# Kernel optimization log

Measured on AMD Instinct MI355X. Metric: run time of the kernel, lower is better.

Reference implementation:

```python
import jax, jax.numpy as jnp
import numpy as np

N_NODES = 50000
N_EDGES = 800000
IN_CH = 128
OUT_CH = 64
HEADS = 4
NEG_SLOPE = 0.2


def setup_inputs() -> dict:
    key = jax.random.key(0)
    k1, k2, k3, k4, k5 = jax.random.split(key, 5)
    x = jax.random.normal(k1, (N_NODES, IN_CH), dtype=jnp.float32)
    edge_index = jax.random.randint(k2, (2, N_EDGES), 0, N_NODES, dtype=jnp.int64)
    # Glorot-ish scaled params
    W = jax.random.normal(k3, (IN_CH, HEADS * OUT_CH), dtype=jnp.float32) * (1.0 / np.sqrt(IN_CH))
    att_src = jax.random.normal(k4, (HEADS, OUT_CH), dtype=jnp.float32) * (1.0 / np.sqrt(OUT_CH))
    att_dst = jax.random.normal(k5, (HEADS, OUT_CH), dtype=jnp.float32) * (1.0 / np.sqrt(OUT_CH))
    bias = jnp.zeros((HEADS * OUT_CH,), dtype=jnp.float32)
    return {"x": x, "edge_index": edge_index, "W": W, "att_src": att_src, "att_dst": att_dst, "bias": bias}


def reference(x, edge_index, W, att_src, att_dst, bias):
    N = x.shape[0]
    H, C = att_src.shape
    # PyG GATConv default add_self_loops=True
    loops = jnp.arange(N, dtype=edge_index.dtype)
    src = jnp.concatenate([edge_index[0], loops])  # message source j
    dst = jnp.concatenate([edge_index[1], loops])  # message target i
    # Linear transform per head: [N, H, C]
    h = (x @ W).reshape(N, H, C)
    # Per-node attention logits: [N, H]
    a_src = jnp.sum(h * att_src[None], axis=-1)
    a_dst = jnp.sum(h * att_dst[None], axis=-1)
    # Per-edge raw score (alpha_src from source node, alpha_dst from target node)
    e = jax.nn.leaky_relu(a_src[src] + a_dst[dst], NEG_SLOPE)  # [E, H]
    # Segment-softmax over incoming edges of each target node
    m = jax.ops.segment_max(e, dst, num_segments=N)  # [N, H]
    m = jnp.where(jnp.isfinite(m), m, 0.0)  # nodes with no edges -> 0
    ex = jnp.exp(e - m[dst])
    denom = jax.ops.segment_sum(ex, dst, num_segments=N)  # [N, H]
    alpha = ex / (denom[dst] + 1e-16)  # [E, H]
    # Weighted aggregate of source features: [N, H, C]
    msg = h[src] * alpha[:, :, None]
    out = jax.ops.segment_sum(msg, dst, num_segments=N)
    # concat=True: flatten heads, add bias
    return out.reshape(N, H * C) + bias
```

## Files before the change

kernel.cpp:

```cpp
#include <hip/hip_runtime.h>

#define N_NODES 50000
#define N_EDGES 800000
#define IN_CH 128
#define OUT_CH 64
#define HEADS 4
#define HC 256
#define NEG_SLOPE 0.2f
#define GEMM_BLOCKS 782
#define COUNT_BLOCKS 782
#define SCAN_BLOCKS 49

#define HB_OFF       0UL
#define WSW_OFF      25600000UL
#define ASRC_OFF     25665536UL
#define ADST_OFF     26465536UL
#define COUNTS_OFF   27265536UL
#define OFFSETS_OFF  27465536UL
#define BSUMS_OFF    27665536UL
#define RANK_OFF     27666560UL
#define SIDX_OFF     30866560UL
#define EXV_OFF      34066560UL

typedef __attribute__((ext_vector_type(8))) short short8;
typedef __attribute__((ext_vector_type(8))) __fp16 f16x8;
typedef __attribute__((ext_vector_type(4))) unsigned uint32x4;
typedef __attribute__((ext_vector_type(4))) float f32x4;
typedef __attribute__((ext_vector_type(2))) __fp16 fp16x2;

__device__ __forceinline__ unsigned f2h2(float a, float b) {
  fp16x2 h = __builtin_amdgcn_cvt_pkrtz(a, b);
  return __builtin_bit_cast(unsigned, h);
}
__device__ __forceinline__ void fma2(float& a0, float& a1, unsigned u, float e) {
  fp16x2 h = __builtin_bit_cast(fp16x2, u);
  a0 = fmaf((float)h.x, e, a0);
  a1 = fmaf((float)h.y, e, a1);
}
__device__ __forceinline__ float lrelu(float e) {
  return e > 0.f ? e : NEG_SLOPE * e;
}

__global__ __launch_bounds__(256) void init_k(const float* __restrict__ W,
                                              unsigned short* __restrict__ Wsw,
                                              int* __restrict__ counts) {
  if (blockIdx.x < 16) {
    int idx = blockIdx.x * 256 + threadIdx.x;
    int l = idx & 63;
    int kc = (idx >> 6) & 3;
    int t = idx >> 8;
    int kbase = kc * 32 + (l >> 4) * 8;
    int col = t * 16 + (l & 15);
    unsigned int p[4];
#pragma unroll
    for (int j = 0; j < 4; ++j) {
      p[j] = f2h2(W[(size_t)(kbase + 2 * j) * HC + col],
                  W[(size_t)(kbase + 2 * j + 1) * HC + col]);
    }
    *(uint4*)(Wsw + (size_t)idx * 8) = make_uint4(p[0], p[1], p[2], p[3]);
  } else {
    int i = (blockIdx.x - 16) * 256 + threadIdx.x;
    if (i < N_NODES) counts[i] = 0;
  }
}

__global__ __launch_bounds__(256) void gemm_count(const float* __restrict__ x,
                                                  const unsigned short* __restrict__ Wsw,
                                                  const float* __restrict__ att_s,
                                                  const float* __restrict__ att_d,
                                                  const int* __restrict__ dstv,
                                                  unsigned short* __restrict__ hb,
                                                  float* __restrict__ a_src,
                                                  float* __restrict__ a_dst,
                                                  int* __restrict__ counts,
                                                  int* __restrict__ rank) {
  __shared__ float Cs[4][16][256];

  if (blockIdx.x >= GEMM_BLOCKS) {
    int base = (blockIdx.x - GEMM_BLOCKS) * 1024 + threadIdx.x;
#pragma unroll
    for (int k = 0; k < 4; ++k) {
      int e = base + k * 256;
      if (e < N_EDGES) rank[e] = atomicAdd(&counts[dstv[e]], 1);
    }
    return;
  }

  const int wave = threadIdx.x >> 6;
  const int l = threadIdx.x & 63;
  const int q = l >> 4;
  const int m = l & 15;
  const int mrow = blockIdx.x * 64 + wave * 16 + m;
  const bool mvalid = mrow < N_NODES;
  const int rc = mvalid ? mrow : (N_NODES - 1);

  f16x8 a[4];
  const float* xr = x + (size_t)rc * IN_CH + q * 8;
#pragma unroll
  for (int kc = 0; kc < 4; ++kc) {
    float4 u = *(const float4*)(xr + kc * 32);
    float4 v = *(const float4*)(xr + kc * 32 + 4);
    uint32x4 t;
    t[0] = f2h2(u.x, u.y);
    t[1] = f2h2(u.z, u.w);
    t[2] = f2h2(v.x, v.y);
    t[3] = f2h2(v.z, v.w);
    a[kc] = __builtin_bit_cast(f16x8, t);
  }

#pragma unroll
  for (int t = 0; t < 16; ++t) {
    f32x4 acc = {0.f, 0.f, 0.f, 0.f};
#pragma unroll
    for (int kc = 0; kc < 4; ++kc) {
      f16x8 b = *(const f16x8*)(Wsw + ((size_t)(t * 4 + kc) * 64 + l) * 8);
      acc = __builtin_amdgcn_mfma_f32_16x16x32_f16(a[kc], b, acc, 0, 0, 0);
    }
#pragma unroll
    for (int r = 0; r < 4; ++r) {
      int row = q * 4 + r;
      Cs[wave][row][(t * 16 + m) ^ (row << 2)] = acc[r];
    }
  }
  __syncthreads();

  float as = 0.f, ad = 0.f;
  unsigned short* hrow = hb + (size_t)mrow * HC + q * 64;
  const int sw = m << 2;
#pragma unroll
  for (int i = 0; i < 8; ++i) {
    int col0 = q * 64 + i * 8;
    float4 c1 = *(const float4*)&Cs[wave][m][(col0) ^ sw];
    float4 c2 = *(const float4*)&Cs[wave][m][(col0 + 4) ^ sw];
    float4 s1 = *(const float4*)(att_s + col0);
    float4 s2 = *(const float4*)(att_s + col0 + 4);
    float4 d1 = *(const float4*)(att_d + col0);
    float4 d2 = *(const float4*)(att_d + col0 + 4);
    as += c1.x * s1.x + c1.y * s1.y + c1.z * s1.z + c1.w * s1.w;
    as += c2.x * s2.x + c2.y * s2.y + c2.z * s2.z + c2.w * s2.w;
    ad += c1.x * d1.x + c1.y * d1.y + c1.z * d1.z + c1.w * d1.w;
    ad += c2.x * d2.x + c2.y * d2.y + c2.z * d2.z + c2.w * d2.w;
    if (mvalid) {
      uint4 p;
      p.x = f2h2(c1.x, c1.y);
      p.y = f2h2(c1.z, c1.w);
      p.z = f2h2(c2.x, c2.y);
      p.w = f2h2(c2.z, c2.w);
      *(uint4*)(hrow + i * 8) = p;
    }
  }
  if (mvalid) {
    a_src[mrow * HEADS + q] = as;
    a_dst[mrow * HEADS + q] = ad;
  }
}

__global__ __launch_bounds__(256) void scan1(const int* __restrict__ counts,
                                             int* __restrict__ offsets,
                                             int* __restrict__ bsums) {
  __shared__ int sd[256];
  const int base = blockIdx.x * 1024;
  const int t = threadIdx.x;
  int v[4];
  int tsum = 0;
#pragma unroll
  for (int k = 0; k < 4; ++k) {
    int i = base + t * 4 + k;
    v[k] = (i < N_NODES) ? counts[i] : 0;
    tsum += v[k];
  }
  sd[t] = tsum;
  __syncthreads();
  for (int off = 1; off < 256; off <<= 1) {
    int xval = (t >= off) ? sd[t - off] : 0;
    __syncthreads();
    sd[t] += xval;
    __syncthreads();
  }
  int excl = sd[t] - tsum;
  int run = excl;
#pragma unroll
  for (int k = 0; k < 4; ++k) {
    int i = base + t * 4 + k;
    if (i < N_NODES) offsets[i] = run;
    run += v[k];
  }
  if (t == 255) bsums[blockIdx.x] = sd[255];
}

__global__ __launch_bounds__(256) void scan23(int* __restrict__ offsets,
                                              const int* __restrict__ bsums) {
  __shared__ int s_add;
  if (threadIdx.x < 64) {
    int lane = threadIdx.x;
    int v = (lane < SCAN_BLOCKS) ? bsums[lane] : 0;
#pragma unroll
    for (int o = 1; o < 64; o <<= 1) {
      int t = __shfl_up(v, o);
      if (lane >= o) v += t;
    }
    int b = blockIdx.x;
    int pre = (b == 0) ? 0 : __shfl(v, b - 1);
    if (lane == 0) s_add = pre;
  }
  __syncthreads();
  const int add = s_add;
  const int base = blockIdx.x * 1024;
  const int t = threadIdx.x;
#pragma unroll
  for (int k = 0; k < 4; ++k) {
    int i = base + t * 4 + k;
    if (i < N_NODES) offsets[i] += add;
  }
}

__global__ __launch_bounds__(256) void scatter_k(const int* __restrict__ src,
                                                 const int* __restrict__ dst,
                                                 const int* __restrict__ rank,
                                                 const int* __restrict__ offsets,
                                                 const float* __restrict__ a_src,
                                                 const float* __restrict__ a_dst,
                                                 int* __restrict__ sidx,
                                                 float* __restrict__ exv) {
  int e = blockIdx.x * 256 + threadIdx.x;
  if (e < N_EDGES) {
    int s = src[e];
    int d = dst[e];
    float4 as = *(const float4*)(a_src + s * 4);
    float4 ad = *(const float4*)(a_dst + d * 4);
    float4 ex;
    ex.x = __expf(lrelu(as.x + ad.x));
    ex.y = __expf(lrelu(as.y + ad.y));
    ex.z = __expf(lrelu(as.z + ad.z));
    ex.w = __expf(lrelu(as.w + ad.w));
    int pos = offsets[d] + rank[e];
    sidx[pos] = s;
    *(float4*)(exv + (size_t)pos * 4) = ex;
  }
}

__global__ __launch_bounds__(256) void aggregate(const unsigned short* __restrict__ hb,
                                                 const float* __restrict__ a_src,
                                                 const float* __restrict__ a_dst,
                                                 const int* __restrict__ counts,
                                                 const int* __restrict__ offsets,
                                                 const int* __restrict__ sidx,
                                                 const float* __restrict__ exv,
                                                 const float* __restrict__ bias,
                                                 float* __restrict__ out) {
  const int node = blockIdx.x * 4 + (threadIdx.x >> 6);
  const int l = threadIdx.x & 63;
  const int g = l >> 4;
  const int q = l & 15;
  const int hd = q >> 2;
  const int cb = q * 32;
  const int deg = counts[node];
  const int start = offsets[node];
  const char* hbase = (const char*)hb;

  float denom = 0.f;
  float acc[16];
#pragma unroll
  for (int k = 0; k < 16; ++k) acc[k] = 0.f;

  for (int j = 0; j + g < deg; j += 8) {
    int i0 = start + j + g;
    bool v1 = (j + g + 4) < deg;
    int i1 = v1 ? (i0 + 4) : i0;
    int s0 = sidx[i0];
    int s1 = sidx[i1];
    float ex0 = exv[(size_t)i0 * 4 + hd];
    float ex1 = v1 ? exv[(size_t)i1 * 4 + hd] : 0.f;
    const char* hp0 = hbase + (size_t)s0 * 512 + cb;
    const char* hp1 = hbase + (size_t)s1 * 512 + cb;
    uint4 A0 = *(const uint4*)hp0;
    uint4 A1 = *(const uint4*)(hp0 + 16);
    uint4 B0 = *(const uint4*)hp1;
    uint4 B1 = *(const uint4*)(hp1 + 16);
    denom += ex0 + ex1;
    fma2(acc[0],  acc[1],  A0.x, ex0);  fma2(acc[2],  acc[3],  A0.y, ex0);
    fma2(acc[4],  acc[5],  A0.z, ex0);  fma2(acc[6],  acc[7],  A0.w, ex0);
    fma2(acc[8],  acc[9],  A1.x, ex0);  fma2(acc[10], acc[11], A1.y, ex0);
    fma2(acc[12], acc[13], A1.z, ex0);  fma2(acc[14], acc[15], A1.w, ex0);
    fma2(acc[0],  acc[1],  B0.x, ex1);  fma2(acc[2],  acc[3],  B0.y, ex1);
    fma2(acc[4],  acc[5],  B0.z, ex1);  fma2(acc[6],  acc[7],  B0.w, ex1);
    fma2(acc[8],  acc[9],  B1.x, ex1);  fma2(acc[10], acc[11], B1.y, ex1);
    fma2(acc[12], acc[13], B1.z, ex1);  fma2(acc[14], acc[15], B1.w, ex1);
  }

  denom += __shfl_xor(denom, 16);
  denom += __shfl_xor(denom, 32);
#pragma unroll
  for (int k = 0; k < 16; ++k) {
    acc[k] += __shfl_xor(acc[k], 16);
    acc[k] += __shfl_xor(acc[k], 32);
  }

  float es = a_src[node * HEADS + hd] + a_dst[node * HEADS + hd];
  float exs = __expf(lrelu(es));
  denom += exs;
  const char* hp = hbase + (size_t)node * 512 + cb;
  uint4 h0 = *(const uint4*)hp;
  uint4 h1 = *(const uint4*)(hp + 16);
  fma2(acc[0],  acc[1],  h0.x, exs);  fma2(acc[2],  acc[3],  h0.y, exs);
  fma2(acc[4],  acc[5],  h0.z, exs);  fma2(acc[6],  acc[7],  h0.w, exs);
  fma2(acc[8],  acc[9],  h1.x, exs);  fma2(acc[10], acc[11], h1.y, exs);
  fma2(acc[12], acc[13], h1.z, exs);  fma2(acc[14], acc[15], h1.w, exs);

  float inv = 1.f / (denom + 1e-16f);
  int c = q * 16 + g * 4;
  float4 bv = *(const float4*)(bias + c);
  float4 o = make_float4(acc[g * 4 + 0] * inv + bv.x, acc[g * 4 + 1] * inv + bv.y,
                         acc[g * 4 + 2] * inv + bv.z, acc[g * 4 + 3] * inv + bv.w);
  *(float4*)(out + (size_t)node * HC + c) = o;
}

extern "C" void kernel_launch(void* const* d_in, const int* in_sizes, int n_in,
                              void* d_out, int out_size, void* d_ws, size_t ws_size,
                              hipStream_t stream) {
  const float* x     = (const float*)d_in[0];
  const int*   ei    = (const int*)d_in[1];
  const float* W     = (const float*)d_in[2];
  const float* att_s = (const float*)d_in[3];
  const float* att_d = (const float*)d_in[4];
  const float* bias  = (const float*)d_in[5];
  float* out = (float*)d_out;

  char* ws = (char*)d_ws;
  unsigned short* hb  = (unsigned short*)(ws + HB_OFF);
  unsigned short* Wsw = (unsigned short*)(ws + WSW_OFF);
  float* a_src  = (float*)(ws + ASRC_OFF);
  float* a_dst  = (float*)(ws + ADST_OFF);
  int* counts   = (int*)(ws + COUNTS_OFF);
  int* offsets  = (int*)(ws + OFFSETS_OFF);
  int* bsums    = (int*)(ws + BSUMS_OFF);
  int* rank     = (int*)(ws + RANK_OFF);
  int* sidx     = (int*)(ws + SIDX_OFF);
  float* exv    = (float*)(ws + EXV_OFF);

  const int* src = ei;
  const int* dst = ei + N_EDGES;

  init_k<<<16 + 196, 256, 0, stream>>>(W, Wsw, counts);
  gemm_count<<<GEMM_BLOCKS + COUNT_BLOCKS, 256, 0, stream>>>(
      x, Wsw, att_s, att_d, dst, hb, a_src, a_dst, counts, rank);
  scan1<<<SCAN_BLOCKS, 256, 0, stream>>>(counts, offsets, bsums);
  scan23<<<SCAN_BLOCKS, 256, 0, stream>>>(offsets, bsums);
  scatter_k<<<3125, 256, 0, stream>>>(src, dst, rank, offsets, a_src, a_dst, sidx, exv);
  aggregate<<<12500, 256, 0, stream>>>(hb, a_src, a_dst, counts, offsets, sidx, exv, bias, out);
}
```

Baseline: 233.5 us.

## Pack per-edge index and fp16 exp weights into one record; halve GEMM LDS tile

The scatter stage now writes one 16-byte record per edge, holding the source index plus the four per-head exp weights packed as fp16, in place of separate index and float4 arrays. Aggregate then reads a single uint4 per edge instead of two scattered loads. The GEMM epilogue is split into two passes over half-width shared-memory tiles, halving LDS use per block to raise occupancy, at the cost of an extra barrier. Storing the exp weights in fp16 loses precision and can overflow for large logits, since there is no max subtraction.

Result: faster. 224.8 us (-3.7%).

```diff
diff --git a/kernel.cpp b/kernel.cpp
--- a/kernel.cpp
+++ b/kernel.cpp
@@ -19,10 +19,8 @@
 #define OFFSETS_OFF  27465536UL
 #define BSUMS_OFF    27665536UL
 #define RANK_OFF     27666560UL
-#define SIDX_OFF     30866560UL
-#define EXV_OFF      34066560UL
-
-typedef __attribute__((ext_vector_type(8))) short short8;
+#define REC_OFF      30866560UL
+
 typedef __attribute__((ext_vector_type(8))) __fp16 f16x8;
 typedef __attribute__((ext_vector_type(4))) unsigned uint32x4;
 typedef __attribute__((ext_vector_type(4))) float f32x4;
@@ -39,6 +37,11 @@
 }
 __device__ __forceinline__ float lrelu(float e) {
   return e > 0.f ? e : NEG_SLOPE * e;
+}
+__device__ __forceinline__ float exhalf(uint4 r, int hd) {
+  unsigned pair = (hd & 2) ? r.z : r.y;
+  fp16x2 h = __builtin_bit_cast(fp16x2, pair);
+  return (hd & 1) ? (float)h.y : (float)h.x;
 }
 
 __global__ __launch_bounds__(256) void init_k(const float* __restrict__ W,
@@ -74,7 +77,7 @@
                                                   float* __restrict__ a_dst,
                                                   int* __restrict__ counts,
                                                   int* __restrict__ rank) {
-  __shared__ float Cs[4][16][256];
+  __shared__ float Cs[4][16][128];
 
   if (blockIdx.x >= GEMM_BLOCKS) {
     int base = (blockIdx.x - GEMM_BLOCKS) * 1024 + threadIdx.x;
@@ -108,45 +111,52 @@
     a[kc] = __builtin_bit_cast(f16x8, t);
   }
 
-#pragma unroll
-  for (int t = 0; t < 16; ++t) {
-    f32x4 acc = {0.f, 0.f, 0.f, 0.f};
-#pragma unroll
-    for (int kc = 0; kc < 4; ++kc) {
-      f16x8 b = *(const f16x8*)(Wsw + ((size_t)(t * 4 + kc) * 64 + l) * 8);
-      acc = __builtin_amdgcn_mfma_f32_16x16x32_f16(a[kc], b, acc, 0, 0, 0);
-    }
-#pragma unroll
-    for (int r = 0; r < 4; ++r) {
-      int row = q * 4 + r;
-      Cs[wave][row][(t * 16 + m) ^ (row << 2)] = acc[r];
-    }
-  }
-  __syncthreads();
-
   float as = 0.f, ad = 0.f;
   unsigned short* hrow = hb + (size_t)mrow * HC + q * 64;
   const int sw = m << 2;
-#pragma unroll
-  for (int i = 0; i < 8; ++i) {
-    int col0 = q * 64 + i * 8;
-    float4 c1 = *(const float4*)&Cs[wave][m][(col0) ^ sw];
-    float4 c2 = *(const float4*)&Cs[wave][m][(col0 + 4) ^ sw];
-    float4 s1 = *(const float4*)(att_s + col0);
-    float4 s2 = *(const float4*)(att_s + col0 + 4);
-    float4 d1 = *(const float4*)(att_d + col0);
-    float4 d2 = *(const float4*)(att_d + col0 + 4);
-    as += c1.x * s1.x + c1.y * s1.y + c1.z * s1.z + c1.w * s1.w;
-    as += c2.x * s2.x + c2.y * s2.y + c2.z * s2.z + c2.w * s2.w;
-    ad += c1.x * d1.x + c1.y * d1.y + c1.z * d1.z + c1.w * d1.w;
-    ad += c2.x * d2.x + c2.y * d2.y + c2.z * d2.z + c2.w * d2.w;
-    if (mvalid) {
-      uint4 p;
-      p.x = f2h2(c1.x, c1.y);
-      p.y = f2h2(c1.z, c1.w);
-      p.z = f2h2(c2.x, c2.y);
-      p.w = f2h2(c2.z, c2.w);
-      *(uint4*)(hrow + i * 8) = p;
+
+#pragma unroll
+  for (int P = 0; P < 2; ++P) {
+    if (P) __syncthreads();
+#pragma unroll
+    for (int tt = 0; tt < 8; ++tt) {
+      int t = ((tt >> 1) << 2) + P * 2 + (tt & 1);
+      f32x4 acc = {0.f, 0.f, 0.f, 0.f};
+#pragma unroll
+      for (int kc = 0; kc < 4; ++kc) {
+        f16x8 b = *(const f16x8*)(Wsw + ((size_t)(t * 4 + kc) * 64 + l) * 8);
+        acc = __builtin_amdgcn_mfma_f32_16x16x32_f16(a[kc], b, acc, 0, 0, 0);
+      }
+#pragma unroll
+      for (int r = 0; r < 4; ++r) {
+        int row = q * 4 + r;
+        Cs[wave][row][(tt * 16 + m) ^ (row << 2)] = acc[r];
+      }
+    }
+    __syncthreads();
+
+#pragma unroll
+    for (int i = 0; i < 4; ++i) {
+      int lcol = q * 32 + i * 8;
+      float4 c1 = *(const float4*)&Cs[wave][m][(lcol) ^ sw];
+      float4 c2 = *(const float4*)&Cs[wave][m][(lcol + 4) ^ sw];
+      int ch = q * 64 + P * 32 + i * 8;
+      float4 s1 = *(const float4*)(att_s + ch);
+      float4 s2 = *(const float4*)(att_s + ch + 4);
+      float4 d1 = *(const float4*)(att_d + ch);
+      float4 d2 = *(const float4*)(att_d + ch + 4);
+      as += c1.x * s1.x + c1.y * s1.y + c1.z * s1.z + c1.w * s1.w;
+      as += c2.x * s2.x + c2.y * s2.y + c2.z * s2.z + c2.w * s2.w;
+      ad += c1.x * d1.x + c1.y * d1.y + c1.z * d1.z + c1.w * d1.w;
+      ad += c2.x * d2.x + c2.y * d2.y + c2.z * d2.z + c2.w * d2.w;
+      if (mvalid) {
+        uint4 p;
+        p.x = f2h2(c1.x, c1.y);
+        p.y = f2h2(c1.z, c1.w);
+        p.z = f2h2(c2.x, c2.y);
+        p.w = f2h2(c2.z, c2.w);
+        *(uint4*)(hrow + P * 32 + i * 8) = p;
+      }
     }
   }
   if (mvalid) {
@@ -220,22 +230,19 @@
                                                  const int* __restrict__ offsets,
                                                  const float* __restrict__ a_src,
                                                  const float* __restrict__ a_dst,
-                                                 int* __restrict__ sidx,
-                                                 float* __restrict__ exv) {
+                                                 uint4* __restrict__ rec) {
   int e = blockIdx.x * 256 + threadIdx.x;
   if (e < N_EDGES) {
     int s = src[e];
     int d = dst[e];
     float4 as = *(const float4*)(a_src + s * 4);
     float4 ad = *(const float4*)(a_dst + d * 4);
-    float4 ex;
-    ex.x = __expf(lrelu(as.x + ad.x));
-    ex.y = __expf(lrelu(as.y + ad.y));
-    ex.z = __expf(lrelu(as.z + ad.z));
-    ex.w = __expf(lrelu(as.w + ad.w));
+    float ex0 = __expf(lrelu(as.x + ad.x));
+    float ex1 = __expf(lrelu(as.y + ad.y));
+    float ex2 = __expf(lrelu(as.z + ad.z));
+    float ex3 = __expf(lrelu(as.w + ad.w));
     int pos = offsets[d] + rank[e];
-    sidx[pos] = s;
-    *(float4*)(exv + (size_t)pos * 4) = ex;
+    rec[pos] = make_uint4((unsigned)s, f2h2(ex0, ex1), f2h2(ex2, ex3), 0u);
   }
 }
 
@@ -244,8 +251,7 @@
                                                  const float* __restrict__ a_dst,
                                                  const int* __restrict__ counts,
                                                  const int* __restrict__ offsets,
-                                                 const int* __restrict__ sidx,
-                                                 const float* __restrict__ exv,
+                                                 const uint4* __restrict__ rec,
                                                  const float* __restrict__ bias,
                                                  float* __restrict__ out) {
   const int node = blockIdx.x * 4 + (threadIdx.x >> 6);
@@ -267,10 +273,12 @@
     int i0 = start + j + g;
     bool v1 = (j + g + 4) < deg;
     int i1 = v1 ? (i0 + 4) : i0;
-    int s0 = sidx[i0];
-    int s1 = sidx[i1];
-    float ex0 = exv[(size_t)i0 * 4 + hd];
-    float ex1 = v1 ? exv[(size_t)i1 * 4 + hd] : 0.f;
+    uint4 r0 = rec[i0];
+    uint4 r1 = rec[i1];
+    int s0 = (int)r0.x;
+    int s1 = (int)r1.x;
+    float ex0 = exhalf(r0, hd);
+    float ex1 = v1 ? exhalf(r1, hd) : 0.f;
     const char* hp0 = hbase + (size_t)s0 * 512 + cb;
     const char* hp1 = hbase + (size_t)s1 * 512 + cb;
     uint4 A0 = *(const uint4*)hp0;
@@ -335,8 +343,7 @@
   int* offsets  = (int*)(ws + OFFSETS_OFF);
   int* bsums    = (int*)(ws + BSUMS_OFF);
   int* rank     = (int*)(ws + RANK_OFF);
-  int* sidx     = (int*)(ws + SIDX_OFF);
-  float* exv    = (float*)(ws + EXV_OFF);
+  uint4* rec    = (uint4*)(ws + REC_OFF);
 
   const int* src = ei;
   const int* dst = ei + N_EDGES;
@@ -346,6 +353,6 @@
       x, Wsw, att_s, att_d, dst, hb, a_src, a_dst, counts, rank);
   scan1<<<SCAN_BLOCKS, 256, 0, stream>>>(counts, offsets, bsums);
   scan23<<<SCAN_BLOCKS, 256, 0, stream>>>(offsets, bsums);
-  scatter_k<<<3125, 256, 0, stream>>>(src, dst, rank, offsets, a_src, a_dst, sidx, exv);
-  aggregate<<<12500, 256, 0, stream>>>(hb, a_src, a_dst, counts, offsets, sidx, exv, bias, out);
-}
+  scatter_k<<<3125, 256, 0, stream>>>(src, dst, rank, offsets, a_src, a_dst, rec);
+  aggregate<<<12500, 256, 0, stream>>>(hb, a_src, a_dst, counts, offsets, rec, bias, out);
+}
```
